# Performance work log

Measured on AMD Instinct MI355X. Metric: run time of the kernel, lower is better.

The kernel has to match this reference:

```python
import jax, jax.numpy as jnp
import numpy as np

B, N_H, N = 32, 16, 64
R, REP, NUM_CLS = 1024, 1024, 117
NUM_ITER = 2
T_LIS, K_LIS, W_LIS = 8.3, 12.0, 10.0

# static pair indices: x in [0,n_h), y in [0,n), x != y  -> M = N_H*N - N_H
_xx, _yy = np.meshgrid(np.arange(N_H), np.arange(N), indexing='ij')
_mask = _xx != _yy
X_IDX = jnp.asarray(_xx[_mask], dtype=jnp.int32)  # [M]
Y_IDX = jnp.asarray(_yy[_mask], dtype=jnp.int32)  # [M]
M = int(_mask.sum())


def lis(x):
    # low-grade suppression
    return T_LIS / (1.0 + jnp.exp(K_LIS - W_LIS * x))


def setup_inputs() -> dict:
    key = jax.random.key(0)
    ks = jax.random.split(key, 18)
    s = 0.02
    p = lambda k, shp: (jax.random.normal(k, shp) * s).astype(jnp.float32)
    box_features = jax.random.normal(ks[0], (B, N, R), dtype=jnp.float32)
    box_coords = jax.random.uniform(ks[1], (B, N, 4), dtype=jnp.float32)
    box_labels = jax.random.randint(ks[2], (B, N), 0, NUM_CLS).astype(jnp.int32)
    box_labels = box_labels.at[:, :N_H].set(0)  # first N_H are humans (human_idx=0)
    box_scores = jax.random.uniform(ks[3], (B, N), dtype=jnp.float32)
    return {
        'box_features': box_features, 'box_coords': box_coords,
        'box_labels': box_labels, 'box_scores': box_scores,
        'W1': p(ks[4], (2 * R, REP)), 'b1': jnp.zeros((REP,), jnp.float32),
        'W2': p(ks[5], (REP, REP // 2)), 'b2': jnp.zeros((REP // 2,), jnp.float32),
        'W3': p(ks[6], (REP // 2, 1)), 'b3': jnp.zeros((1,), jnp.float32),
        'Ws': p(ks[7], (R, REP)), 'bs': jnp.zeros((REP,), jnp.float32),
        'Wo': p(ks[8], (R, REP)), 'bo': jnp.zeros((REP,), jnp.float32),
        'Wsu': p(ks[9], (R + REP, R)),
        'Wou': p(ks[10], (R + REP, R)),
    }


def reference(box_features, box_coords, box_labels, box_scores,
              W1, b1, W2, b2, W3, b3, Ws, bs, Wo, bo, Wsu, Wou):
    def per_image(enc, coords, labels, scores):
        # enc: [N, R]
        A = jnp.zeros((N_H, N), enc.dtype)
        for _ in range(NUM_ITER):
            pe = jnp.concatenate([enc[X_IDX], enc[Y_IDX]], axis=1)  # [M, 2R]
            h = jax.nn.relu(pe @ W1 + b1)
            h = jax.nn.relu(h @ W2 + b2)
            w = (h @ W3 + b3)[:, 0]  # [M]
            A = jnp.zeros((N_H, N), enc.dtype).at[X_IDX, Y_IDX].set(jax.nn.sigmoid(w))
            msg_h = A @ jax.nn.relu(enc @ Wo + bo)                      # [N_H, REP]
            enc_h = jnp.concatenate([enc[:N_H], msg_h], axis=1) @ Wsu  # [N_H, R]
            enc = enc.at[:N_H].set(enc_h)
            msg_o = A.T @ jax.nn.relu(enc_h @ Ws + bs)                  # [N, REP]
            enc = jnp.concatenate([enc, msg_o], axis=1) @ Wou           # [N, R]
        pair = jnp.concatenate([enc[X_IDX], enc[Y_IDX]], axis=1)  # [M, 2R]
        prod = lis(scores[X_IDX]) * lis(scores[Y_IDX])            # [M]
        # identity object_class_to_target_class: class c -> [c]
        prior = jnp.zeros((M, NUM_CLS), enc.dtype).at[jnp.arange(M), labels[Y_IDX]].set(prod)
        prior = A[X_IDX, Y_IDX][:, None] * prior
        return pair, coords[X_IDX], coords[Y_IDX], prior

    pair, bh, bo_, prior = jax.vmap(per_image)(box_features, box_coords, box_labels, box_scores)
    return (pair.reshape(B * M, 2 * R), bh, bo_, prior.reshape(B * M, NUM_CLS))
```

## Files before the change

### kernel.cpp

```cpp
#include <hip/hip_runtime.h>

#define B_   32
#define N_   64
#define NH   16
#define R_   1024
#define REP  1024
#define M_   1008
#define BM   (B_ * M_)
#define NCLS 117

#define MD_DIRECT 0
#define MD_CC1    2
#define MD_CC2    3

typedef short bhalf8 __attribute__((ext_vector_type(8)));
typedef float f32x4  __attribute__((ext_vector_type(4)));

typedef __attribute__((address_space(3))) void       lds_t;
typedef const __attribute__((address_space(1))) void gbl_t;
__device__ __forceinline__ void gld16(const void* g, void* l)
{
    __builtin_amdgcn_global_load_lds((gbl_t*)g, (lds_t*)l, 16, 0, 0);
}

__device__ __forceinline__ unsigned short f2bf(float f)
{
    union { float f; unsigned int u; } x; x.f = f;
    unsigned int r = x.u + 0x7FFFu + ((x.u >> 16) & 1u);
    return (unsigned short)(r >> 16);
}
__device__ __forceinline__ float bf2f(unsigned short u)
{
    union { unsigned int i; float f; } x; x.i = ((unsigned int)u) << 16; return x.f;
}

__device__ __forceinline__ unsigned int addrelu2(unsigned int a, unsigned int b)
{
    union { unsigned int u; float f; } la, ha, lb, hb;
    la.u = a << 16;          ha.u = a & 0xffff0000u;
    lb.u = b << 16;          hb.u = b & 0xffff0000u;
    float lo = fmaxf(la.f + lb.f, 0.f);
    float hi = fmaxf(ha.f + hb.f, 0.f);
    unsigned int r;
    asm("v_cvt_pk_bf16_f32 %0, %1, %2" : "=v"(r) : "v"(lo), "v"(hi));
    return r;
}

__device__ __forceinline__ void wait_vm(int n)
{
    if (n >= 8)      asm volatile("s_waitcnt vmcnt(8)" ::: "memory");
    else if (n == 6) asm volatile("s_waitcnt vmcnt(6)" ::: "memory");
    else if (n == 4) asm volatile("s_waitcnt vmcnt(4)" ::: "memory");
    else if (n == 2) asm volatile("s_waitcnt vmcnt(2)" ::: "memory");
    else             asm volatile("s_waitcnt vmcnt(0)" ::: "memory");
}
__device__ __forceinline__ void wait_vm_lgkm(int n)
{
    if (n >= 12)      asm volatile("s_waitcnt vmcnt(12) lgkmcnt(0)" ::: "memory");
    else if (n >= 10) asm volatile("s_waitcnt vmcnt(10) lgkmcnt(0)" ::: "memory");
    else              asm volatile("s_waitcnt vmcnt(8) lgkmcnt(0)" ::: "memory");
}

__device__ __forceinline__ void tr32(const float* in, unsigned short* out,
                                     int K, int N, int local)
{
    __shared__ float t[32][33];
    int kb = K >> 5;
    int k0 = (local % kb) * 32, n0 = (local / kb) * 32;
    int tx = threadIdx.x & 31, ty = threadIdx.x >> 5;
#pragma unroll
    for (int r = 0; r < 4; ++r)
        t[ty + r * 8][tx] = in[(size_t)(k0 + ty + r * 8) * N + n0 + tx];
    __syncthreads();
#pragma unroll
    for (int r = 0; r < 4; ++r)
        out[(size_t)(n0 + ty + r * 8) * K + k0 + tx] = f2bf(t[tx][ty + r * 8]);
}

__global__ __launch_bounds__(256)
void prep_all(const float* __restrict__ W1, const float* __restrict__ W2,
              const float* __restrict__ Wo, const float* __restrict__ Ws,
              const float* __restrict__ Wsu, const float* __restrict__ Wou,
              const float* __restrict__ bo_, const float* __restrict__ b1_,
              const float* __restrict__ feat,
              unsigned short* __restrict__ Wfused, unsigned short* __restrict__ W2t,
              unsigned short* __restrict__ Wst, unsigned short* __restrict__ Wsut,
              unsigned short* __restrict__ Wout, float* __restrict__ biasFull,
              unsigned short* __restrict__ enc0bf)
{
    int bx = blockIdx.x;
    if      (bx < 1024) tr32(W1 + 1024 * 1024, Wfused,               1024, 1024, bx);
    else if (bx < 2048) tr32(Wo,               Wfused + 1024 * 1024, 1024, 1024, bx - 1024);
    else if (bx < 3072) tr32(W1,               Wfused + 2048 * 1024, 1024, 1024, bx - 2048);
    else if (bx < 3584) tr32(W2,  W2t,  1024, 512,  bx - 3072);
    else if (bx < 4608) tr32(Ws,  Wst,  1024, 1024, bx - 3584);
    else if (bx < 6656) tr32(Wsu, Wsut, 2048, 1024, bx - 4608);
    else if (bx < 8704) tr32(Wou, Wout, 2048, 1024, bx - 6656);
    else if (bx < 8716) {
        int c = (bx - 8704) * 256 + threadIdx.x;
        float v = 0.f;
        if (c >= 2048)      v = b1_[c - 2048];
        else if (c >= 1024) v = bo_[c - 1024];
        biasFull[c] = v;
    } else {
        int i = (bx - 8716) * 256 + threadIdx.x;
        float4 a = ((const float4*)feat)[2 * i];
        float4 b = ((const float4*)feat)[2 * i + 1];
        uint4 o;
        o.x = (unsigned)f2bf(a.x) | ((unsigned)f2bf(a.y) << 16);
        o.y = (unsigned)f2bf(a.z) | ((unsigned)f2bf(a.w) << 16);
        o.z = (unsigned)f2bf(b.x) | ((unsigned)f2bf(b.y) << 16);
        o.w = (unsigned)f2bf(b.z) | ((unsigned)f2bf(b.w) << 16);
        ((uint4*)enc0bf)[i] = o;
    }
}

__global__ __launch_bounds__(256)
void gemm_uvgo(const unsigned short* __restrict__ enc,
               const unsigned short* __restrict__ Wf,
               const float* __restrict__ biasFull, unsigned short* __restrict__ XX)
{
    __shared__ unsigned short As[3][128 * 32];
    __shared__ unsigned short Bs[3][128 * 32];
    const int tid  = threadIdx.x;
    const int lane = tid & 63, wave = tid >> 6;
    const int wm = wave & 1, wn = wave >> 1;
    const int l15 = lane & 15, lk = lane >> 4;
    const int row0 = blockIdx.y * 128, col0 = blockIdx.x * 128;
    const int kq = (lane & 3) * 8;

    const unsigned short* pA[2];
    const unsigned short* pB[2];
    int ldsOff[2];
#pragma unroll
    for (int i = 0; i < 2; ++i) {
        int tr = wave * 32 + (lane >> 2) + i * 16;
        pA[i]  = enc + (size_t)(row0 + tr) * 1024 + kq;
        pB[i]  = Wf  + (size_t)(col0 + tr) * 1024 + kq;
        ldsOff[i] = wave * 1024 + i * 512 + lane * 8;
    }

#define STG_UV(slot, k0) do {                          \
        gld16(pA[0] + (k0), &As[slot][ldsOff[0]]);     \
        gld16(pA[1] + (k0), &As[slot][ldsOff[1]]);     \
        gld16(pB[0] + (k0), &Bs[slot][ldsOff[0]]);     \
        gld16(pB[1] + (k0), &Bs[slot][ldsOff[1]]); } while (0)

    f32x4 acc[4][4];
#pragma unroll
    for (int i = 0; i < 4; ++i)
#pragma unroll
    for (int j = 0; j < 4; ++j) acc[i][j] = (f32x4)0.f;

    STG_UV(0, 0);
    STG_UV(1, 32);
    for (int t = 0; t < 32; ++t) {
        const int slot = t % 3;
        if (t + 2 < 32) STG_UV((t + 2) % 3, (t + 2) * 32);
        wait_vm(t < 30 ? 8 : (t == 30 ? 4 : 0));
        __builtin_amdgcn_s_barrier();
        __builtin_amdgcn_sched_barrier(0);
        bhalf8 af[4], bf4[4];
#pragma unroll
        for (int mt = 0; mt < 4; ++mt)
            af[mt] = *(bhalf8*)&As[slot][(wm * 64 + mt * 16 + l15) * 32 + lk * 8];
#pragma unroll
        for (int nt = 0; nt < 4; ++nt)
            bf4[nt] = *(bhalf8*)&Bs[slot][(wn * 64 + nt * 16 + l15) * 32 + lk * 8];
#pragma unroll
        for (int mt = 0; mt < 4; ++mt)
#pragma unroll
        for (int nt = 0; nt < 4; ++nt)
            acc[mt][nt] = __builtin_amdgcn_mfma_f32_16x16x32_bf16(af[mt], bf4[nt],
                                                                  acc[mt][nt], 0, 0, 0);
        __builtin_amdgcn_sched_barrier(0);
        __builtin_amdgcn_s_barrier();
    }
#undef STG_UV

#pragma unroll
    for (int mt = 0; mt < 4; ++mt)
#pragma unroll
    for (int r = 0; r < 4; ++r) {
        int row = row0 + wm * 64 + mt * 16 + lk * 4 + r;
#pragma unroll
        for (int nt = 0; nt < 4; ++nt) {
            int col = col0 + wn * 64 + nt * 16 + l15;
            float v = acc[mt][nt][r] + biasFull[col];
            if ((col >> 10) == 1) v = fmaxf(v, 0.f);
            XX[(size_t)row * 3072 + col] = f2bf(v);
        }
    }
}

__global__ __launch_bounds__(256)
void pair_bf(const unsigned short* __restrict__ XX,
             const unsigned short* __restrict__ W2t, const float* __restrict__ b2,
             const float* __restrict__ W3f, float* __restrict__ wpart)
{
    __shared__ unsigned short As[128 * 32];
    __shared__ unsigned short Bs[3][128 * 32];
    __shared__ float red[2][128];
    const int tid  = threadIdx.x;
    const int lane = tid & 63, wave = tid >> 6;
    const int wm = wave & 1, wn = wave >> 1;
    const int l15 = lane & 15, lk = lane >> 4;
    const int row0 = blockIdx.y * 128, col0 = blockIdx.x * 128;

    const int srow = tid >> 1, skh = tid & 1;
    int rg = row0 + srow;
    int b  = rg / M_, m = rg % M_;
    int x  = m / 63, jj = m % 63;
    int y  = jj + (jj >= x ? 1 : 0);
    const unsigned short* Up = XX + ((size_t)(b * 64 + x)) * 3072 + 2048 + skh * 16;
    const unsigned short* Vp = XX + ((size_t)(b * 64 + y)) * 3072 + skh * 16;
    unsigned short* AsW = As + srow * 32 + skh * 16;

    const int kq = (lane & 3) * 8;
    const unsigned short* pB[2];
    int bO[2];
#pragma unroll
    for (int i = 0; i < 2; ++i) {
        int tr = wave * 32 + (lane >> 2) + i * 16;
        pB[i] = W2t + (size_t)(col0 + tr) * REP + kq;
        bO[i] = wave * 1024 + i * 512 + lane * 8;
    }

#define STG_B(slot, k0) do {                        \
        gld16(pB[0] + (k0), &Bs[slot][bO[0]]);      \
        gld16(pB[1] + (k0), &Bs[slot][bO[1]]); } while (0)

    f32x4 acc[4][4];
#pragma unroll
    for (int i = 0; i < 4; ++i)
#pragma unroll
    for (int j = 0; j < 4; ++j) acc[i][j] = (f32x4)0.f;

    uint4 cu0 = *(const uint4*)(Up);
    uint4 cu1 = *(const uint4*)(Up + 8);
    uint4 cv0 = *(const uint4*)(Vp);
    uint4 cv1 = *(const uint4*)(Vp + 8);
    STG_B(0, 0);
    STG_B(1, 32);

    for (int t = 0; t < 32; ++t) {
        const int slot = t % 3;
        const int kn = (t + 1 < 32) ? (t + 1) * 32 : 0;
        uint4 nu0 = *(const uint4*)(Up + kn);
        uint4 nu1 = *(const uint4*)(Up + kn + 8);
        uint4 nv0 = *(const uint4*)(Vp + kn);
        uint4 nv1 = *(const uint4*)(Vp + kn + 8);
        if (t + 2 < 32) STG_B((t + 2) % 3, (t + 2) * 32);

        uint4 h0, h1;
        h0.x = addrelu2(cu0.x, cv0.x); h0.y = addrelu2(cu0.y, cv0.y);
        h0.z = addrelu2(cu0.z, cv0.z); h0.w = addrelu2(cu0.w, cv0.w);
        h1.x = addrelu2(cu1.x, cv1.x); h1.y = addrelu2(cu1.y, cv1.y);
        h1.z = addrelu2(cu1.z, cv1.z); h1.w = addrelu2(cu1.w, cv1.w);
        *(uint4*)(AsW)     = h0;
        *(uint4*)(AsW + 8) = h1;

        wait_vm_lgkm(t == 0 ? 8 : (t < 30 ? 12 : (t == 30 ? 10 : 8)));
        __builtin_amdgcn_s_barrier();
        __builtin_amdgcn_sched_barrier(0);
        bhalf8 af[4], bf4[4];
#pragma unroll
        for (int mt = 0; mt < 4; ++mt)
            af[mt] = *(bhalf8*)&As[(wm * 64 + mt * 16 + l15) * 32 + lk * 8];
#pragma unroll
        for (int nt = 0; nt < 4; ++nt)
            bf4[nt] = *(bhalf8*)&Bs[slot][(wn * 64 + nt * 16 + l15) * 32 + lk * 8];
#pragma unroll
        for (int mt = 0; mt < 4; ++mt)
#pragma unroll
        for (int nt = 0; nt < 4; ++nt)
            acc[mt][nt] = __builtin_amdgcn_mfma_f32_16x16x32_bf16(af[mt], bf4[nt],
                                                                  acc[mt][nt], 0, 0, 0);
        __builtin_amdgcn_sched_barrier(0);
        __builtin_amdgcn_s_barrier();
        cu0 = nu0; cu1 = nu1; cv0 = nv0; cv1 = nv1;
    }
#undef STG_B

    float b2v[4], w3v[4];
#pragma unroll
    for (int nt = 0; nt < 4; ++nt) {
        int col = col0 + wn * 64 + nt * 16 + l15;
        b2v[nt] = b2[col];
        w3v[nt] = W3f[col];
    }
#pragma unroll
    for (int mt = 0; mt < 4; ++mt)
#pragma unroll
    for (int r = 0; r < 4; ++r) {
        int rloc = wm * 64 + mt * 16 + lk * 4 + r;
        float p = 0.f;
#pragma unroll
        for (int nt = 0; nt < 4; ++nt)
            p += fmaxf(acc[mt][nt][r] + b2v[nt], 0.f) * w3v[nt];
        p += __shfl_xor(p, 1); p += __shfl_xor(p, 2);
        p += __shfl_xor(p, 4); p += __shfl_xor(p, 8);
        if (l15 == 0) red[wn][rloc] = p;
    }
    __syncthreads();
    if (tid < 128)
        wpart[blockIdx.x * BM + row0 + tid] = red[0][tid] + red[1][tid];
}

__device__ __forceinline__ void compute_A(const float* __restrict__ wpart, float b3v,
                                          int b, float* Al, int t)
{
    for (int i = t; i < NH * N_; i += 128) {
        int y = i & 63, x = i >> 6;
        float v = 0.f;
        if (y != x) {
            int j = y - (y > x ? 1 : 0);
            int r = b * M_ + x * 63 + j;
            float s = b3v + wpart[r] + wpart[BM + r] + wpart[2 * BM + r] + wpart[3 * BM + r];
            v = 1.f / (1.f + expf(-s));
        }
        Al[i] = v;
    }
}

__global__ __launch_bounds__(128)
void msgh_kernel(const float* __restrict__ wpart, const float* __restrict__ b3,
                 const unsigned short* __restrict__ XX,
                 unsigned short* __restrict__ msgh, float* __restrict__ Aw)
{
    __shared__ float Al[NH * N_];
    __shared__ float Gl[N_][128];
    int b = blockIdx.x, c0 = blockIdx.y * 128, t = threadIdx.x;
    compute_A(wpart, b3[0], b, Al, t);
    for (int y = 0; y < N_; ++y)
        Gl[y][t] = bf2f(XX[((size_t)(b * 64 + y)) * 3072 + 1024 + c0 + t]);
    __syncthreads();
    if (blockIdx.y == 0)
        for (int i = t; i < NH * N_; i += 128) Aw[b * NH * N_ + i] = Al[i];
    for (int x = 0; x < NH; ++x) {
        float s = 0.f;
#pragma unroll 8
        for (int y = 0; y < N_; ++y) s += Al[x * N_ + y] * Gl[y][t];
        msgh[((size_t)(b * NH + x)) * REP + c0 + t] = f2bf(s);
    }
}

__global__ __launch_bounds__(128)
void msgo_kernel(const float* __restrict__ wpart, const float* __restrict__ b3,
                 const unsigned short* __restrict__ Gs, unsigned short* __restrict__ msgo)
{
    __shared__ float Al[NH * N_];
    __shared__ float Gl[NH][128];
    int b = blockIdx.x, c0 = blockIdx.y * 128, t = threadIdx.x;
    compute_A(wpart, b3[0], b, Al, t);
    for (int x = 0; x < NH; ++x)
        Gl[x][t] = bf2f(Gs[((size_t)(b * NH + x)) * REP + c0 + t]);
    __syncthreads();
    for (int y = 0; y < N_; ++y) {
        float s = 0.f;
#pragma unroll
        for (int x = 0; x < NH; ++x) s += Al[x * N_ + y] * Gl[x][t];
        msgo[((size_t)(b * N_ + y)) * REP + c0 + t] = f2bf(s);
    }
}

__global__ __launch_bounds__(256)
void gemm_small(const unsigned short* __restrict__ A1, const unsigned short* __restrict__ A2,
                const unsigned short* __restrict__ A3, const unsigned short* __restrict__ Bt,
                const float* __restrict__ bias, float* __restrict__ Cf,
                unsigned short* __restrict__ Cb, int K, int Nc, int doRelu, int mode)
{
    __shared__ unsigned short As[4][64 * 32];
    __shared__ unsigned short Bs[4][64 * 32];
    const int tid  = threadIdx.x;
    const int lane = tid & 63, wave = tid >> 6;
    const int wr = wave & 1, wc = wave >> 1;
    const int l15 = lane & 15, lk = lane >> 4;
    const int row0 = blockIdx.y * 64, col0 = blockIdx.x * 64;
    const int kq = (lane & 3) * 8;

    int tr = wave * 16 + (lane >> 2);
    int rr = row0 + tr;
    const unsigned short* p1;
    const unsigned short* p2 = nullptr;
    if (mode == MD_DIRECT) {
        p1 = A1 + (size_t)rr * K;
    } else if (mode == MD_CC1) {
        int b = rr >> 4, x = rr & 15;
        p1 = A1 + (size_t)(b * 64 + x) * 1024;
        p2 = A2 + (size_t)rr * 1024 - 1024;
    } else {
        int b = rr >> 6, n = rr & 63;
        p1 = (n < 16) ? A3 + (size_t)(b * 16 + n) * 1024
                      : A1 + (size_t)rr * 1024;
        p2 = A2 + (size_t)rr * 1024 - 1024;
    }
    const unsigned short* pA1 = p1 + kq;
    const unsigned short* pA2 = p2 ? p2 + kq : nullptr;
    const unsigned short* pB  = Bt + (size_t)(col0 + tr) * K + kq;
    const int stO = wave * 512 + lane * 8;
    const int kSw = (mode != MD_DIRECT) ? 1024 : K;
    const int NT = K >> 5;

#define STG_MID(slot, k0) do {                                  \
        const unsigned short* ap = ((k0) < kSw) ? pA1 : pA2;    \
        gld16(ap + (k0), &As[slot][stO]);                       \
        gld16(pB + (k0), &Bs[slot][stO]); } while (0)

    f32x4 acc[2][2];
#pragma unroll
    for (int i = 0; i < 2; ++i)
#pragma unroll
    for (int j = 0; j < 2; ++j) acc[i][j] = (f32x4)0.f;

    STG_MID(0, 0);
    STG_MID(1, 32);
    STG_MID(2, 64);
    for (int t = 0; t < NT; ++t) {
        const int slot = t & 3;
        if (t + 3 < NT) STG_MID((t + 3) & 3, (t + 3) * 32);
        int rem = NT - 1 - t;
        wait_vm(rem >= 3 ? 6 : rem * 2);
        __builtin_amdgcn_s_barrier();
        __builtin_amdgcn_sched_barrier(0);
        bhalf8 af[2], bf4[2];
#pragma unroll
        for (int mt = 0; mt < 2; ++mt)
            af[mt] = *(bhalf8*)&As[slot][(wr * 32 + mt * 16 + l15) * 32 + lk * 8];
#pragma unroll
        for (int nt = 0; nt < 2; ++nt)
            bf4[nt] = *(bhalf8*)&Bs[slot][(wc * 32 + nt * 16 + l15) * 32 + lk * 8];
#pragma unroll
        for (int mt = 0; mt < 2; ++mt)
#pragma unroll
        for (int nt = 0; nt < 2; ++nt)
            acc[mt][nt] = __builtin_amdgcn_mfma_f32_16x16x32_bf16(af[mt], bf4[nt],
                                                                  acc[mt][nt], 0, 0, 0);
        __builtin_amdgcn_sched_barrier(0);
        __builtin_amdgcn_s_barrier();
    }
#undef STG_MID

#pragma unroll
    for (int mt = 0; mt < 2; ++mt)
#pragma unroll
    for (int r = 0; r < 4; ++r) {
        int row = row0 + wr * 32 + mt * 16 + lk * 4 + r;
#pragma unroll
        for (int nt = 0; nt < 2; ++nt) {
            int col = col0 + wc * 32 + nt * 16 + l15;
            float v = acc[mt][nt][r];
            if (bias) v += bias[col];
            if (doRelu) v = fmaxf(v, 0.f);
            if (Cf) Cf[(size_t)row * Nc + col] = v;
            if (Cb) Cb[(size_t)row * Nc + col] = f2bf(v);
        }
    }
}

__device__ __forceinline__ float lis_f(float x)
{
    return 8.3f / (1.f + expf(12.f - 10.f * x));
}

__global__ __launch_bounds__(256)
void outputs_all(const float* __restrict__ enc, const float* __restrict__ coords,
                 const float* __restrict__ Aw, const int* __restrict__ labels,
                 const float* __restrict__ scores,
                 float* __restrict__ out0, float* __restrict__ out1,
                 float* __restrict__ out2, float* __restrict__ out3)
{
    int bx = blockIdx.x;
    if (bx < 64512) {
        int i = bx * 256 + threadIdx.x;
        int r = i >> 9, q = i & 511;
        int b = r / M_, m = r % M_;
        int x = m / 63, j = m % 63;
        int y = j + (j >= x ? 1 : 0);
        const float4* e4 = (const float4*)enc;
        float4 v = (q < 256) ? e4[(b * 64 + x) * 256 + q]
                             : e4[(b * 64 + y) * 256 + (q - 256)];
        ((float4*)out0)[i] = v;
    } else if (bx < 64638) {
        int r = (bx - 64512) * 256 + threadIdx.x;
        int b = r / M_, m = r % M_;
        int x = m / 63, j = m % 63;
        int y = j + (j >= x ? 1 : 0);
        const float4* c4 = (const float4*)coords;
        ((float4*)out1)[r] = c4[b * 64 + x];
        ((float4*)out2)[r] = c4[b * 64 + y];
    } else {
        int i = (bx - 64638) * 256 + threadIdx.x;
        int r = i / NCLS, c = i % NCLS;
        int b = r / M_, m = r % M_;
        int x = m / 63, j = m % 63;
        int y = j + (j >= x ? 1 : 0);
        int lab = labels[b * 64 + y];
        float val = 0.f;
        if (c == lab) {
            float sx = scores[b * 64 + x], sy = scores[b * 64 + y];
            val = Aw[(b * NH + x) * N_ + y] * lis_f(sx) * lis_f(sy);
        }
        out3[i] = val;
    }
}

extern "C" void kernel_launch(void* const* d_in, const int* in_sizes, int n_in,
                              void* d_out, int out_size, void* d_ws, size_t ws_size,
                              hipStream_t stream)
{
    const float* box_features = (const float*)d_in[0];
    const float* box_coords   = (const float*)d_in[1];
    const int*   box_labels   = (const int*)d_in[2];
    const float* box_scores   = (const float*)d_in[3];
    const float* W1  = (const float*)d_in[4];
    const float* b1  = (const float*)d_in[5];
    const float* W2  = (const float*)d_in[6];
    const float* b2  = (const float*)d_in[7];
    const float* W3  = (const float*)d_in[8];
    const float* b3  = (const float*)d_in[9];
    const float* Ws  = (const float*)d_in[10];
    const float* bs  = (const float*)d_in[11];
    const float* Wo  = (const float*)d_in[12];
    const float* bo  = (const float*)d_in[13];
    const float* Wsu = (const float*)d_in[14];
    const float* Wou = (const float*)d_in[15];

    float* wsf  = (float*)d_ws;
    float* encA = wsf;           wsf += (size_t)B_ * N_ * R_;
    float* wpart= wsf;           wsf += (size_t)4 * BM;
    float* Aw   = wsf;           wsf += (size_t)B_ * NH * N_;
    float* biasFull = wsf;       wsf += 3072;

    unsigned short* wsu = (unsigned short*)wsf;
    unsigned short* enc0bf = wsu;  wsu += (size_t)B_ * N_ * R_;
    unsigned short* encIbf = wsu;  wsu += (size_t)B_ * N_ * R_;
    unsigned short* XX     = wsu;  wsu += (size_t)B_ * N_ * 3072;
    unsigned short* msghbf = wsu;  wsu += (size_t)B_ * NH * REP;
    unsigned short* enchbf = wsu;  wsu += (size_t)B_ * NH * R_;
    unsigned short* Gsbf   = wsu;  wsu += (size_t)B_ * NH * REP;
    unsigned short* msgobf = wsu;  wsu += (size_t)B_ * N_ * REP;
    unsigned short* Wfused = wsu;  wsu += (size_t)3072 * 1024;
    unsigned short* W2t    = wsu;  wsu += (size_t)512 * 1024;
    unsigned short* Wst    = wsu;  wsu += (size_t)1024 * 1024;
    unsigned short* Wsut   = wsu;  wsu += (size_t)1024 * 2048;
    unsigned short* Wout   = wsu;  wsu += (size_t)1024 * 2048;

    float* out0 = (float*)d_out;
    float* out1 = out0 + (size_t)BM * 2048;
    float* out2 = out1 + (size_t)BM * 4;
    float* out3 = out2 + (size_t)BM * 4;

    prep_all<<<9740, 256, 0, stream>>>(W1, W2, Wo, Ws, Wsu, Wou, bo, b1, box_features,
                                       Wfused, W2t, Wst, Wsut, Wout, biasFull, enc0bf);

    for (int it = 0; it < 2; ++it) {
        const unsigned short* enc = (it == 0) ? enc0bf : encIbf;
        gemm_uvgo<<<dim3(24, 16), 256, 0, stream>>>(enc, Wfused, biasFull, XX);
        pair_bf<<<dim3(4, 252), 256, 0, stream>>>(XX, W2t, b2, W3, wpart);
        msgh_kernel<<<dim3(32, 8), 128, 0, stream>>>(wpart, b3, XX, msghbf, Aw);
        gemm_small<<<dim3(16, 8), 256, 0, stream>>>(enc, msghbf, nullptr, Wsut, nullptr,
                                                    nullptr, enchbf, 2048, 1024, 0, MD_CC1);
        gemm_small<<<dim3(16, 8), 256, 0, stream>>>(enchbf, nullptr, nullptr, Wst, bs,
                                                    nullptr, Gsbf, 1024, 1024, 1, MD_DIRECT);
        msgo_kernel<<<dim3(32, 8), 128, 0, stream>>>(wpart, b3, Gsbf, msgobf);
        gemm_small<<<dim3(16, 32), 256, 0, stream>>>(enc, msgobf, enchbf, Wout, nullptr,
                                                     (it == 1) ? encA : nullptr,
                                                     (it == 0) ? encIbf : nullptr,
                                                     1024 * 2, 1024, 0, MD_CC2);
    }

    outputs_all<<<79380, 256, 0, stream>>>(encA, box_coords, Aw, box_labels, box_scores,
                                           out0, out1, out2, out3);
}
```

Before: 751.5 us.

## Fuse msg_o aggregation into final update GEMM via reassociated A^T(Gs·Wbottom)

Removes the separate msgo kernel and its bf16 round-trip buffer by reassociating A^T·Gs·W_bottom. Each block computes Gs·W_bottom with extra MFMAs and applies the 64x16 A^T mix in fp32 registers in the epilogue. The new gemm_cc2 uses a 3-stage pipeline that stages three tiles per step. It recomputes A from wpart in-kernel and in outputs_all instead of storing Aw. This saves a launch and a global-memory pass. In exchange, each of the 16 column blocks per image recomputes the 16-row Gs·W product, and the change adds LDS pressure (~50KB).

Result: faster. 718.7 us (-4.4%).

```diff
diff --git a/kernel.cpp b/kernel.cpp
--- a/kernel.cpp
+++ b/kernel.cpp
@@ -11,7 +11,6 @@
 
 #define MD_DIRECT 0
 #define MD_CC1    2
-#define MD_CC2    3
 
 typedef short bhalf8 __attribute__((ext_vector_type(8)));
 typedef float f32x4  __attribute__((ext_vector_type(4)));
@@ -51,6 +50,7 @@
     if (n >= 8)      asm volatile("s_waitcnt vmcnt(8)" ::: "memory");
     else if (n == 6) asm volatile("s_waitcnt vmcnt(6)" ::: "memory");
     else if (n == 4) asm volatile("s_waitcnt vmcnt(4)" ::: "memory");
+    else if (n == 3) asm volatile("s_waitcnt vmcnt(3)" ::: "memory");
     else if (n == 2) asm volatile("s_waitcnt vmcnt(2)" ::: "memory");
     else             asm volatile("s_waitcnt vmcnt(0)" ::: "memory");
 }
@@ -326,7 +326,7 @@
 __global__ __launch_bounds__(128)
 void msgh_kernel(const float* __restrict__ wpart, const float* __restrict__ b3,
                  const unsigned short* __restrict__ XX,
-                 unsigned short* __restrict__ msgh, float* __restrict__ Aw)
+                 unsigned short* __restrict__ msgh)
 {
     __shared__ float Al[NH * N_];
     __shared__ float Gl[N_][128];
@@ -335,8 +335,6 @@
     for (int y = 0; y < N_; ++y)
         Gl[y][t] = bf2f(XX[((size_t)(b * 64 + y)) * 3072 + 1024 + c0 + t]);
     __syncthreads();
-    if (blockIdx.y == 0)
-        for (int i = t; i < NH * N_; i += 128) Aw[b * NH * N_ + i] = Al[i];
     for (int x = 0; x < NH; ++x) {
         float s = 0.f;
 #pragma unroll 8
@@ -345,29 +343,9 @@
     }
 }
 
-__global__ __launch_bounds__(128)
-void msgo_kernel(const float* __restrict__ wpart, const float* __restrict__ b3,
-                 const unsigned short* __restrict__ Gs, unsigned short* __restrict__ msgo)
-{
-    __shared__ float Al[NH * N_];
-    __shared__ float Gl[NH][128];
-    int b = blockIdx.x, c0 = blockIdx.y * 128, t = threadIdx.x;
-    compute_A(wpart, b3[0], b, Al, t);
-    for (int x = 0; x < NH; ++x)
-        Gl[x][t] = bf2f(Gs[((size_t)(b * NH + x)) * REP + c0 + t]);
-    __syncthreads();
-    for (int y = 0; y < N_; ++y) {
-        float s = 0.f;
-#pragma unroll
-        for (int x = 0; x < NH; ++x) s += Al[x * N_ + y] * Gl[x][t];
-        msgo[((size_t)(b * N_ + y)) * REP + c0 + t] = f2bf(s);
-    }
-}
-
 __global__ __launch_bounds__(256)
 void gemm_small(const unsigned short* __restrict__ A1, const unsigned short* __restrict__ A2,
-                const unsigned short* __restrict__ A3, const unsigned short* __restrict__ Bt,
-                const float* __restrict__ bias, float* __restrict__ Cf,
+                const unsigned short* __restrict__ Bt, const float* __restrict__ bias,
                 unsigned short* __restrict__ Cb, int K, int Nc, int doRelu, int mode)
 {
     __shared__ unsigned short As[4][64 * 32];
@@ -385,14 +363,9 @@
     const unsigned short* p2 = nullptr;
     if (mode == MD_DIRECT) {
         p1 = A1 + (size_t)rr * K;
-    } else if (mode == MD_CC1) {
+    } else {
         int b = rr >> 4, x = rr & 15;
         p1 = A1 + (size_t)(b * 64 + x) * 1024;
-        p2 = A2 + (size_t)rr * 1024 - 1024;
-    } else {
-        int b = rr >> 6, n = rr & 63;
-        p1 = (n < 16) ? A3 + (size_t)(b * 16 + n) * 1024
-                      : A1 + (size_t)rr * 1024;
         p2 = A2 + (size_t)rr * 1024 - 1024;
     }
     const unsigned short* pA1 = p1 + kq;
@@ -452,8 +425,143 @@
             float v = acc[mt][nt][r];
             if (bias) v += bias[col];
             if (doRelu) v = fmaxf(v, 0.f);
-            if (Cf) Cf[(size_t)row * Nc + col] = v;
-            if (Cb) Cb[(size_t)row * Nc + col] = f2bf(v);
+            Cb[(size_t)row * Nc + col] = f2bf(v);
+        }
+    }
+}
+
+__global__ __launch_bounds__(256)
+void gemm_cc2(const unsigned short* __restrict__ enc,
+              const unsigned short* __restrict__ ench,
+              const unsigned short* __restrict__ Gs,
+              const unsigned short* __restrict__ Wout,
+              const float* __restrict__ wpart, const float* __restrict__ b3,
+              float* __restrict__ Cf, unsigned short* __restrict__ Cb)
+{
+    __shared__ unsigned short As[3][64 * 32];
+    __shared__ unsigned short Bt[3][64 * 32];
+    __shared__ unsigned short Bb[3][64 * 32];
+    __shared__ unsigned short GsL[16][1056];
+    __shared__ float Al[16][64];
+    __shared__ float gsl[16][68];
+
+    const int tid  = threadIdx.x;
+    const int lane = tid & 63, wave = tid >> 6;
+    const int wr = wave & 1, wc = wave >> 1;
+    const int l15 = lane & 15, lk = lane >> 4;
+    const int b = blockIdx.y, col0 = blockIdx.x * 64;
+    const int kq = (lane & 3) * 8;
+
+#pragma unroll
+    for (int j = 0; j < 8; ++j) {
+        int idx = j * 256 + tid;
+        int row = idx >> 7, c8 = (idx & 127) * 8;
+        uint4 v = *(const uint4*)(Gs + ((size_t)(b * 16 + row)) * 1024 + c8);
+        *(uint4*)&GsL[row][c8] = v;
+    }
+    float b3v = b3[0];
+#pragma unroll
+    for (int j = 0; j < 4; ++j) {
+        int i = j * 256 + tid;
+        int y = i & 63, x = i >> 6;
+        float v = 0.f;
+        if (y != x) {
+            int jj = y - (y > x ? 1 : 0);
+            int r = b * M_ + x * 63 + jj;
+            float s = b3v + wpart[r] + wpart[BM + r] + wpart[2 * BM + r] + wpart[3 * BM + r];
+            v = 1.f / (1.f + expf(-s));
+        }
+        Al[x][y] = v;
+    }
+    asm volatile("s_waitcnt lgkmcnt(0)" ::: "memory");
+
+    int tr = wave * 16 + (lane >> 2);
+    const unsigned short* pA = (tr < 16 ? ench + ((size_t)(b * 16 + tr)) * 1024
+                                        : enc  + ((size_t)(b * 64 + tr)) * 1024) + kq;
+    const unsigned short* pBt = Wout + (size_t)(col0 + tr) * 2048 + kq;
+    const unsigned short* pBb = pBt + 1024;
+    const int stO = wave * 512 + lane * 8;
+
+#define STG_C2(slot, k0) do {                      \
+        gld16(pA  + (k0), &As[slot][stO]);         \
+        gld16(pBt + (k0), &Bt[slot][stO]);         \
+        gld16(pBb + (k0), &Bb[slot][stO]); } while (0)
+
+    f32x4 acc[2][2];
+    f32x4 accg[2];
+#pragma unroll
+    for (int i = 0; i < 2; ++i) {
+        accg[i] = (f32x4)0.f;
+#pragma unroll
+        for (int j = 0; j < 2; ++j) acc[i][j] = (f32x4)0.f;
+    }
+
+    STG_C2(0, 0);
+    STG_C2(1, 32);
+    for (int t = 0; t < 32; ++t) {
+        const int slot = t % 3;
+        if (t + 2 < 32) STG_C2((t + 2) % 3, (t + 2) * 32);
+        wait_vm(t < 30 ? 6 : (t == 30 ? 3 : 0));
+        __builtin_amdgcn_s_barrier();
+        __builtin_amdgcn_sched_barrier(0);
+        bhalf8 af[2], bt4[2], bb4[2], ags;
+#pragma unroll
+        for (int mt = 0; mt < 2; ++mt)
+            af[mt] = *(bhalf8*)&As[slot][(wr * 32 + mt * 16 + l15) * 32 + lk * 8];
+#pragma unroll
+        for (int nt = 0; nt < 2; ++nt) {
+            bt4[nt] = *(bhalf8*)&Bt[slot][(wc * 32 + nt * 16 + l15) * 32 + lk * 8];
+            bb4[nt] = *(bhalf8*)&Bb[slot][(wc * 32 + nt * 16 + l15) * 32 + lk * 8];
+        }
+        ags = *(bhalf8*)&GsL[l15][t * 32 + lk * 8];
+#pragma unroll
+        for (int mt = 0; mt < 2; ++mt)
+#pragma unroll
+        for (int nt = 0; nt < 2; ++nt)
+            acc[mt][nt] = __builtin_amdgcn_mfma_f32_16x16x32_bf16(af[mt], bt4[nt],
+                                                                  acc[mt][nt], 0, 0, 0);
+#pragma unroll
+        for (int nt = 0; nt < 2; ++nt)
+            accg[nt] = __builtin_amdgcn_mfma_f32_16x16x32_bf16(ags, bb4[nt],
+                                                               accg[nt], 0, 0, 0);
+        __builtin_amdgcn_sched_barrier(0);
+        __builtin_amdgcn_s_barrier();
+    }
+#undef STG_C2
+
+    if (wr == 0) {
+#pragma unroll
+        for (int nt = 0; nt < 2; ++nt)
+#pragma unroll
+        for (int r = 0; r < 4; ++r)
+            gsl[lk * 4 + r][wc * 32 + nt * 16 + l15] = accg[nt][r];
+    }
+    __syncthreads();
+
+#pragma unroll
+    for (int x = 0; x < 16; ++x) {
+        float g0 = gsl[x][wc * 32 + l15];
+        float g1 = gsl[x][wc * 32 + 16 + l15];
+#pragma unroll
+        for (int mt = 0; mt < 2; ++mt)
+#pragma unroll
+        for (int r = 0; r < 4; ++r) {
+            float a = Al[x][wr * 32 + mt * 16 + lk * 4 + r];
+            acc[mt][0][r] += a * g0;
+            acc[mt][1][r] += a * g1;
+        }
+    }
+#pragma unroll
+    for (int mt = 0; mt < 2; ++mt)
+#pragma unroll
+    for (int r = 0; r < 4; ++r) {
+        size_t row = (size_t)b * 64 + wr * 32 + mt * 16 + lk * 4 + r;
+#pragma unroll
+        for (int nt = 0; nt < 2; ++nt) {
+            int col = col0 + wc * 32 + nt * 16 + l15;
+            float v = acc[mt][nt][r];
+            if (Cf) Cf[row * 1024 + col] = v;
+            else    Cb[row * 1024 + col] = f2bf(v);
         }
     }
 }
@@ -465,8 +573,8 @@
 
 __global__ __launch_bounds__(256)
 void outputs_all(const float* __restrict__ enc, const float* __restrict__ coords,
-                 const float* __restrict__ Aw, const int* __restrict__ labels,
-                 const float* __restrict__ scores,
+                 const float* __restrict__ wpart, const float* __restrict__ b3,
+                 const int* __restrict__ labels, const float* __restrict__ scores,
                  float* __restrict__ out0, float* __restrict__ out1,
                  float* __restrict__ out2, float* __restrict__ out3)
 {
@@ -498,8 +606,10 @@
         int lab = labels[b * 64 + y];
         float val = 0.f;
         if (c == lab) {
+            float w = b3[0] + wpart[r] + wpart[BM + r] + wpart[2 * BM + r] + wpart[3 * BM + r];
+            float A = 1.f / (1.f + expf(-w));
             float sx = scores[b * 64 + x], sy = scores[b * 64 + y];
-            val = Aw[(b * NH + x) * N_ + y] * lis_f(sx) * lis_f(sy);
+            val = A * lis_f(sx) * lis_f(sy);
         }
         out3[i] = val;
     }
@@ -529,7 +639,6 @@
     float* wsf  = (float*)d_ws;
     float* encA = wsf;           wsf += (size_t)B_ * N_ * R_;
     float* wpart= wsf;           wsf += (size_t)4 * BM;
-    float* Aw   = wsf;           wsf += (size_t)B_ * NH * N_;
     float* biasFull = wsf;       wsf += 3072;
 
     unsigned short* wsu = (unsigned short*)wsf;
@@ -539,7 +648,6 @@
     unsigned short* msghbf = wsu;  wsu += (size_t)B_ * NH * REP;
     unsigned short* enchbf = wsu;  wsu += (size_t)B_ * NH * R_;
     unsigned short* Gsbf   = wsu;  wsu += (size_t)B_ * NH * REP;
-    unsigned short* msgobf = wsu;  wsu += (size_t)B_ * N_ * REP;
     unsigned short* Wfused = wsu;  wsu += (size_t)3072 * 1024;
     unsigned short* W2t    = wsu;  wsu += (size_t)512 * 1024;
     unsigned short* Wst    = wsu;  wsu += (size_t)1024 * 1024;
@@ -558,18 +666,17 @@
         const unsigned short* enc = (it == 0) ? enc0bf : encIbf;
         gemm_uvgo<<<dim3(24, 16), 256, 0, stream>>>(enc, Wfused, biasFull, XX);
         pair_bf<<<dim3(4, 252), 256, 0, stream>>>(XX, W2t, b2, W3, wpart);
-        msgh_kernel<<<dim3(32, 8), 128, 0, stream>>>(wpart, b3, XX, msghbf, Aw);
-        gemm_small<<<dim3(16, 8), 256, 0, stream>>>(enc, msghbf, nullptr, Wsut, nullptr,
-                                                    nullptr, enchbf, 2048, 1024, 0, MD_CC1);
-        gemm_small<<<dim3(16, 8), 256, 0, stream>>>(enchbf, nullptr, nullptr, Wst, bs,
-                                                    nullptr, Gsbf, 1024, 1024, 1, MD_DIRECT);
-        msgo_kernel<<<dim3(32, 8), 128, 0, stream>>>(wpart, b3, Gsbf, msgobf);
-        gemm_small<<<dim3(16, 32), 256, 0, stream>>>(enc, msgobf, enchbf, Wout, nullptr,
-                                                     (it == 1) ? encA : nullptr,
-                                                     (it == 0) ? encIbf : nullptr,
-                                                     1024 * 2, 1024, 0, MD_CC2);
-    }
-
-    outputs_all<<<79380, 256, 0, stream>>>(encA, box_coords, Aw, box_labels, box_scores,
+        msgh_kernel<<<dim3(32, 8), 128, 0, stream>>>(wpart, b3, XX, msghbf);
+        gemm_small<<<dim3(16, 8), 256, 0, stream>>>(enc, msghbf, Wsut, nullptr,
+                                                    enchbf, 2048, 1024, 0, MD_CC1);
+        gemm_small<<<dim3(16, 8), 256, 0, stream>>>(enchbf, nullptr, Wst, bs,
+                                                    Gsbf, 1024, 1024, 1, MD_DIRECT);
+        gemm_cc2<<<dim3(16, 32), 256, 0, stream>>>(enc, enchbf, Gsbf, Wout, wpart, b3,
+                                                   (it == 1) ? encA : nullptr,
+                                                   (it == 0) ? encIbf : nullptr);
+    }
+
+    outputs_all<<<79380, 256, 0, stream>>>(encA, box_coords, wpart, b3,
+                                           box_labels, box_scores,
                                            out0, out1, out2, out3);
 }
```
